# Kernel tuning notes

Hardware: AMD Instinct MI355X
Metric: run time of the kernel (lower is better)

The kernel has to match this reference:

```python
import jax, jax.numpy as jnp
import numpy as np

SEQ_LEN, BATCH, DIM = 128, 128, 1024

def setup_inputs() -> dict:
    key = jax.random.key(0)
    k1, k2, k3, k4 = jax.random.split(key, 4)
    scale = 1.0 / np.sqrt(DIM)
    return {
        "x": jax.random.normal(k1, (SEQ_LEN, BATCH, DIM), dtype=jnp.float32),
        "h0": jax.random.normal(k2, (BATCH, DIM), dtype=jnp.float32),
        "Wx": jax.random.normal(k3, (DIM, DIM), dtype=jnp.float32) * scale,
        "Wh": jax.random.normal(k4, (DIM, DIM), dtype=jnp.float32) * scale,
        "b": jnp.zeros((DIM,), dtype=jnp.float32),
    }

def reference(x, h0, Wx, Wh, b):
    # Vanilla tanh RNN cell scanned over seq_len (dropout is identity at keep_prob=1).
    # Precompute the input projection for all timesteps in one big GEMM.
    xp = jnp.einsum('sbi,ij->sbj', x, Wx) + b  # [S, B, H]
    def step(h, xp_t):
        h_new = jnp.tanh(xp_t + h @ Wh)
        return h_new, h_new
    _, hs = jax.lax.scan(step, h0, xp)
    return hs  # [seq_len, batch, hidden]: stacked hidden states
```

## Files before the change

kernel.cpp:

```cpp
#include <hip/hip_runtime.h>
#include <math.h>


#define DIM 1024
#define BATCH 128
#define SEQ 128
#define BD (BATCH * DIM)
#define NBLK 128
#define GRP 16
#define HSTR 1032
#define FLAGSTR 16
#define XNB 256
#define HXGRP 16384

typedef __attribute__((ext_vector_type(8))) short bf16x8;
typedef __attribute__((ext_vector_type(4))) float f32x4;

static __device__ __forceinline__ unsigned short f2bf_rne(float f) {
    unsigned u = __builtin_bit_cast(unsigned, f);
    unsigned r = (u + 0x7FFFu + ((u >> 16) & 1u)) >> 16;
    return (unsigned short)r;
}
static __device__ __forceinline__ float bf2f(unsigned short h) {
    return __builtin_bit_cast(float, ((unsigned)h) << 16);
}

__global__ __launch_bounds__(512) void xp_pers(
    const float* __restrict__ x,
    const float* __restrict__ Wx,
    const float* __restrict__ bias,
    float* __restrict__ out)
{
    __shared__ unsigned short hHi[16 * HSTR];
    __shared__ unsigned short hLo[16 * HSTR];
    __shared__ f32x4 redS[256];

    const int tid = threadIdx.x;
    const int bid = blockIdx.x;
    const int tg  = bid >> 7;
    const int bt  = (bid >> 4) & 7;
    const int ct  = bid & 15;
    const int B0  = bt * 16;
    const int Cb  = ct * 64;
    const int NT  = SEQ / 2;

    const int w = tid >> 6;
    const int l = tid & 63;
    const int n = l & 15;
    const int q = l >> 4;
    const int cb = Cb + (w >> 1) * 16;
    const int K0 = (w & 1) * 512;

    bf16x8 Bhi[16], Blo[16];
    #pragma unroll
    for (int s = 0; s < 16; ++s) {
        bf16x8 hi, lo;
        #pragma unroll
        for (int j = 0; j < 8; ++j) {
            const int k = K0 + 32 * s + q * 8 + j;
            const float wv = Wx[(size_t)k * DIM + cb + n];
            const unsigned short h16 = f2bf_rne(wv);
            hi[j] = (short)h16;
            lo[j] = (short)f2bf_rne(wv - bf2f(h16));
        }
        Bhi[s] = hi;
        Blo[s] = lo;
    }

    const float bv = bias[cb + n];

    const int sr = tid >> 5;
    const int su = tid & 31;

    {
        const float* xT = x + (size_t)(tg * NT) * BD + (size_t)B0 * DIM;
        const unsigned long long* srow =
            (const unsigned long long*)(xT + (size_t)sr * DIM);
        unsigned short* dh = &hHi[sr * HSTR];
        unsigned short* dl = &hLo[sr * HSTR];
        #pragma unroll
        for (int i = 0; i < 16; ++i) {
            const unsigned long long v = srow[su + 32 * i];
            const float f0 = __builtin_bit_cast(float, (unsigned)(v & 0xFFFFFFFFull));
            const float f1 = __builtin_bit_cast(float, (unsigned)(v >> 32));
            const unsigned short h0 = f2bf_rne(f0);
            const unsigned short h1 = f2bf_rne(f1);
            const unsigned short l0 = f2bf_rne(f0 - bf2f(h0));
            const unsigned short l1 = f2bf_rne(f1 - bf2f(h1));
            *(unsigned*)(dh + 2 * (su + 32 * i)) = (unsigned)h0 | ((unsigned)h1 << 16);
            *(unsigned*)(dl + 2 * (su + 32 * i)) = (unsigned)l0 | ((unsigned)l1 << 16);
        }
    }

    for (int tt = 0; tt < NT; ++tt) {
        const int t = tg * NT + tt;
        float* outT = out + (size_t)t * BD;

        __syncthreads();

        unsigned long long xr[16];
        if (tt + 1 < NT) {
            const float* xN = x + (size_t)(t + 1) * BD + (size_t)B0 * DIM;
            const unsigned long long* srow =
                (const unsigned long long*)(xN + (size_t)sr * DIM);
            #pragma unroll
            for (int i = 0; i < 16; ++i) xr[i] = srow[su + 32 * i];
        }

        f32x4 acc = {0.f, 0.f, 0.f, 0.f};
        {
            const unsigned short* rh = &hHi[(l & 15) * HSTR + K0];
            const unsigned short* rl = &hLo[(l & 15) * HSTR + K0];
            #pragma unroll
            for (int s = 0; s < 16; ++s) {
                const bf16x8 ah = *(const bf16x8*)(rh + 32 * s + 8 * q);
                const bf16x8 al = *(const bf16x8*)(rl + 32 * s + 8 * q);
                acc = __builtin_amdgcn_mfma_f32_16x16x32_bf16(ah, Bhi[s], acc, 0, 0, 0);
                acc = __builtin_amdgcn_mfma_f32_16x16x32_bf16(al, Bhi[s], acc, 0, 0, 0);
                acc = __builtin_amdgcn_mfma_f32_16x16x32_bf16(ah, Blo[s], acc, 0, 0, 0);
            }
        }

        if (w & 1) redS[(w >> 1) * 64 + l] = acc;
        __syncthreads();

        if (!(w & 1)) {
            const f32x4 p = redS[(w >> 1) * 64 + l];
            #pragma unroll
            for (int i = 0; i < 4; ++i)
                outT[(size_t)(B0 + q * 4 + i) * DIM + cb + n] = acc[i] + p[i] + bv;
        }

        if (tt + 1 < NT) {
            unsigned short* dh = &hHi[sr * HSTR];
            unsigned short* dl = &hLo[sr * HSTR];
            #pragma unroll
            for (int i = 0; i < 16; ++i) {
                const unsigned long long v = xr[i];
                const float f0 = __builtin_bit_cast(float, (unsigned)(v & 0xFFFFFFFFull));
                const float f1 = __builtin_bit_cast(float, (unsigned)(v >> 32));
                const unsigned short h0 = f2bf_rne(f0);
                const unsigned short h1 = f2bf_rne(f1);
                const unsigned short l0 = f2bf_rne(f0 - bf2f(h0));
                const unsigned short l1 = f2bf_rne(f1 - bf2f(h1));
                *(unsigned*)(dh + 2 * (su + 32 * i)) = (unsigned)h0 | ((unsigned)h1 << 16);
                *(unsigned*)(dl + 2 * (su + 32 * i)) = (unsigned)l0 | ((unsigned)l1 << 16);
            }
        }
    }
}

__global__ __launch_bounds__(512) void rnn_scan(
    const float* __restrict__ h0,
    const float* __restrict__ Wh,
    float* out,
    unsigned* flags,
    unsigned short* hX)
{
    __shared__ unsigned short hS[16 * HSTR];
    __shared__ f32x4 redS[256];

    const int tid = threadIdx.x;
    const int bid = blockIdx.x;
    const int bt  = bid >> 4;
    const int ct  = bid & 15;
    const int B0  = bt * 16;
    const int Cb  = ct * 64;

    const int w = tid >> 6;
    const int l = tid & 63;
    const int n = l & 15;
    const int q = l >> 4;
    const int cb = Cb + (w >> 1) * 16;
    const int K0 = (w & 1) * 512;

    bf16x8 Bhi[16], Blo[16];
    #pragma unroll
    for (int s = 0; s < 16; ++s) {
        bf16x8 hi, lo;
        #pragma unroll
        for (int j = 0; j < 8; ++j) {
            const int k = K0 + 32 * s + q * 8 + j;
            const float wv = Wh[(size_t)k * DIM + cb + n];
            const unsigned short h16 = f2bf_rne(wv);
            hi[j] = (short)h16;
            lo[j] = (short)f2bf_rne(wv - bf2f(h16));
        }
        Bhi[s] = hi;
        Blo[s] = lo;
    }

    const int sr = tid >> 5;
    const int su = tid & 31;
    const int qq = tid & 3;
    const int c0 = (tid >> 2) & 127;

    for (int t = 0; t < SEQ; ++t) {
        float* outT = out + (size_t)t * BD;

        float xpv[4];
        if (!(w & 1)) {
            #pragma unroll
            for (int i = 0; i < 4; ++i)
                xpv[i] = __builtin_nontemporal_load(
                    &outT[(size_t)(B0 + q * 4 + i) * DIM + cb + n]);
        }

        if (t == 0) {
            const float* hsrc = h0 + (size_t)B0 * DIM;
            const unsigned long long* srow =
                (const unsigned long long*)(hsrc + (size_t)sr * DIM);
            unsigned short* drow = &hS[sr * HSTR];
            #pragma unroll
            for (int i = 0; i < 16; ++i) {
                const unsigned long long v = srow[su + 32 * i];
                const float f0 = __builtin_bit_cast(float, (unsigned)(v & 0xFFFFFFFFull));
                const float f1 = __builtin_bit_cast(float, (unsigned)(v >> 32));
                const unsigned pk =
                    (unsigned)f2bf_rne(f0) | ((unsigned)f2bf_rne(f1) << 16);
                *(unsigned*)(drow + 2 * (su + 32 * i)) = pk;
            }
        } else {
            const unsigned short* gX = hX + (size_t)((t - 1) & 1) * (8 * HXGRP)
                                          + (size_t)bt * HXGRP;
            #pragma unroll
            for (int half = 0; half < 2; ++half) {
                const int cp = c0 + half * 128;
                unsigned long long L[4];
                #pragma unroll
                for (int cc = 0; cc < 4; ++cc)
                    L[cc] = __hip_atomic_load(
                        (const unsigned long long*)(gX + (size_t)(4 * cp + cc) * 16 + qq * 4),
                        __ATOMIC_RELAXED, __HIP_MEMORY_SCOPE_AGENT);
                #pragma unroll
                for (int i = 0; i < 2; ++i) {
                    const unsigned a0 = (unsigned)(L[0] >> (32 * i));
                    const unsigned a1 = (unsigned)(L[1] >> (32 * i));
                    const unsigned a2 = (unsigned)(L[2] >> (32 * i));
                    const unsigned a3 = (unsigned)(L[3] >> (32 * i));
                    const unsigned r0w0 = (a0 & 0xFFFFu) | (a1 << 16);
                    const unsigned r0w1 = (a2 & 0xFFFFu) | (a3 << 16);
                    const unsigned r1w0 = (a0 >> 16) | (a1 & 0xFFFF0000u);
                    const unsigned r1w1 = (a2 >> 16) | (a3 & 0xFFFF0000u);
                    *(unsigned long long*)&hS[(4 * qq + 2 * i) * HSTR + 4 * cp] =
                        (unsigned long long)r0w0 | ((unsigned long long)r0w1 << 32);
                    *(unsigned long long*)&hS[(4 * qq + 2 * i + 1) * HSTR + 4 * cp] =
                        (unsigned long long)r1w0 | ((unsigned long long)r1w1 << 32);
                }
            }
        }

        __syncthreads();

        f32x4 acc = {0.f, 0.f, 0.f, 0.f};
        {
            const unsigned short* hrow = &hS[(l & 15) * HSTR + K0];
            #pragma unroll
            for (int s = 0; s < 16; ++s) {
                const bf16x8 a = *(const bf16x8*)(hrow + 32 * s + 8 * q);
                acc = __builtin_amdgcn_mfma_f32_16x16x32_bf16(a, Bhi[s], acc, 0, 0, 0);
                acc = __builtin_amdgcn_mfma_f32_16x16x32_bf16(a, Blo[s], acc, 0, 0, 0);
            }
        }

        if (w & 1) redS[(w >> 1) * 64 + l] = acc;
        __syncthreads();

        if (!(w & 1)) {
            const f32x4 p = redS[(w >> 1) * 64 + l];
            float v0 = tanhf(acc[0] + p[0] + xpv[0]);
            float v1 = tanhf(acc[1] + p[1] + xpv[1]);
            float v2 = tanhf(acc[2] + p[2] + xpv[2]);
            float v3 = tanhf(acc[3] + p[3] + xpv[3]);

            const unsigned p0 = (unsigned)f2bf_rne(v0) | ((unsigned)f2bf_rne(v1) << 16);
            const unsigned p1 = (unsigned)f2bf_rne(v2) | ((unsigned)f2bf_rne(v3) << 16);
            unsigned short* gW = hX + (size_t)(t & 1) * (8 * HXGRP) + (size_t)bt * HXGRP;
            __hip_atomic_store(
                (unsigned long long*)(gW + (size_t)(cb + n) * 16 + q * 4),
                (unsigned long long)p0 | ((unsigned long long)p1 << 32),
                __ATOMIC_RELAXED, __HIP_MEMORY_SCOPE_AGENT);

            __builtin_nontemporal_store(v0, &outT[(size_t)(B0 + q * 4 + 0) * DIM + cb + n]);
            __builtin_nontemporal_store(v1, &outT[(size_t)(B0 + q * 4 + 1) * DIM + cb + n]);
            __builtin_nontemporal_store(v2, &outT[(size_t)(B0 + q * 4 + 2) * DIM + cb + n]);
            __builtin_nontemporal_store(v3, &outT[(size_t)(B0 + q * 4 + 3) * DIM + cb + n]);
        }

        if (t < SEQ - 1) {
            asm volatile("s_waitcnt vmcnt(0)" ::: "memory");
            __syncthreads();
            if (tid == 0)
                __hip_atomic_store(&flags[bid * FLAGSTR], (unsigned)(t + 1),
                                   __ATOMIC_RELAXED, __HIP_MEMORY_SCOPE_AGENT);
            if (tid < GRP) {
                const unsigned* slot = &flags[(bt * GRP + tid) * FLAGSTR];
                while (__hip_atomic_load(slot, __ATOMIC_RELAXED,
                                         __HIP_MEMORY_SCOPE_AGENT) < (unsigned)(t + 1))
                    __builtin_amdgcn_s_sleep(2);
            }
            __syncthreads();
        }
    }
}

extern "C" void kernel_launch(void* const* d_in, const int* in_sizes, int n_in,
                              void* d_out, int out_size, void* d_ws, size_t ws_size,
                              hipStream_t stream) {
    const float* x  = (const float*)d_in[0];
    const float* h0 = (const float*)d_in[1];
    const float* Wx = (const float*)d_in[2];
    const float* Wh = (const float*)d_in[3];
    const float* b  = (const float*)d_in[4];
    float* out = (float*)d_out;
    unsigned* flags = (unsigned*)d_ws;
    unsigned short* hX = (unsigned short*)((char*)d_ws + 8192);

    hipMemsetAsync(d_ws, 0, NBLK * FLAGSTR * sizeof(unsigned), stream);

    xp_pers<<<dim3(XNB), dim3(512), 0, stream>>>(x, Wx, b, out);

    rnn_scan<<<dim3(NBLK), dim3(512), 0, stream>>>(h0, Wh, out, flags, hX);
}
```

Before: 800.6 us.

## Fuse input projection and recurrent scan into one kernel with flag-based overlap

Merges the input-projection producer and the recurrent scan into one persistent launch of 384 blocks. The 256 projection blocks write xp timestep by timestep, interleaving timesteps between the two groups, and publish per-block progress flags. The 128 scan blocks spin on those flags before reading xp, so the projection runs underneath the sequential recurrence instead of before it. The projection's hi/lo weight split is also moved from within-wave to across wave pairs, and the scan now signals its flag before its output stores. The cost is more register pressure and dependence on all 384 blocks being co-resident; without that the spin-waits could deadlock.

```diff
diff --git a/kernel.cpp b/kernel.cpp
--- a/kernel.cpp
+++ b/kernel.cpp
@@ -6,11 +6,12 @@
 #define BATCH 128
 #define SEQ 128
 #define BD (BATCH * DIM)
-#define NBLK 128
+#define XNB 256
+#define SNB 128
+#define TNB 384
 #define GRP 16
 #define HSTR 1032
 #define FLAGSTR 16
-#define XNB 256
 #define HXGRP 16384
 
 typedef __attribute__((ext_vector_type(8))) short bf16x8;
@@ -25,281 +26,267 @@
     return __builtin_bit_cast(float, ((unsigned)h) << 16);
 }
 
-__global__ __launch_bounds__(512) void xp_pers(
+__global__ __launch_bounds__(512, 4) void rnn_fused(
     const float* __restrict__ x,
+    const float* __restrict__ h0,
     const float* __restrict__ Wx,
+    const float* __restrict__ Wh,
     const float* __restrict__ bias,
-    float* __restrict__ out)
+    float* out,
+    unsigned* scanflags,
+    unsigned* xpflags,
+    unsigned short* hX)
 {
-    __shared__ unsigned short hHi[16 * HSTR];
-    __shared__ unsigned short hLo[16 * HSTR];
+    __shared__ unsigned short smA[16 * HSTR];
+    __shared__ unsigned short smB[16 * HSTR];
     __shared__ f32x4 redS[256];
 
     const int tid = threadIdx.x;
-    const int bid = blockIdx.x;
-    const int tg  = bid >> 7;
-    const int bt  = (bid >> 4) & 7;
-    const int ct  = bid & 15;
-    const int B0  = bt * 16;
-    const int Cb  = ct * 64;
-    const int NT  = SEQ / 2;
-
+    const int gid = blockIdx.x;
     const int w = tid >> 6;
     const int l = tid & 63;
     const int n = l & 15;
     const int q = l >> 4;
-    const int cb = Cb + (w >> 1) * 16;
-    const int K0 = (w & 1) * 512;
-
-    bf16x8 Bhi[16], Blo[16];
-    #pragma unroll
-    for (int s = 0; s < 16; ++s) {
-        bf16x8 hi, lo;
-        #pragma unroll
-        for (int j = 0; j < 8; ++j) {
-            const int k = K0 + 32 * s + q * 8 + j;
-            const float wv = Wx[(size_t)k * DIM + cb + n];
-            const unsigned short h16 = f2bf_rne(wv);
-            hi[j] = (short)h16;
-            lo[j] = (short)f2bf_rne(wv - bf2f(h16));
-        }
-        Bhi[s] = hi;
-        Blo[s] = lo;
-    }
-
-    const float bv = bias[cb + n];
 
     const int sr = tid >> 5;
     const int su = tid & 31;
 
-    {
-        const float* xT = x + (size_t)(tg * NT) * BD + (size_t)B0 * DIM;
-        const unsigned long long* srow =
-            (const unsigned long long*)(xT + (size_t)sr * DIM);
-        unsigned short* dh = &hHi[sr * HSTR];
-        unsigned short* dl = &hLo[sr * HSTR];
+    if (gid < XNB) {
+        const int tg = gid >> 7;
+        const int bt = (gid >> 4) & 7;
+        const int ct = gid & 15;
+        const int B0 = bt * 16;
+        const int Cb = ct * 64;
+        const int cb = Cb + (w >> 1) * 16;
+        const int role = w & 1;
+
+        bf16x8 Bfr[32];
         #pragma unroll
-        for (int i = 0; i < 16; ++i) {
-            const unsigned long long v = srow[su + 32 * i];
-            const float f0 = __builtin_bit_cast(float, (unsigned)(v & 0xFFFFFFFFull));
-            const float f1 = __builtin_bit_cast(float, (unsigned)(v >> 32));
-            const unsigned short h0 = f2bf_rne(f0);
-            const unsigned short h1 = f2bf_rne(f1);
-            const unsigned short l0 = f2bf_rne(f0 - bf2f(h0));
-            const unsigned short l1 = f2bf_rne(f1 - bf2f(h1));
-            *(unsigned*)(dh + 2 * (su + 32 * i)) = (unsigned)h0 | ((unsigned)h1 << 16);
-            *(unsigned*)(dl + 2 * (su + 32 * i)) = (unsigned)l0 | ((unsigned)l1 << 16);
+        for (int s = 0; s < 32; ++s) {
+            bf16x8 fr;
+            #pragma unroll
+            for (int j = 0; j < 8; ++j) {
+                const int k = 32 * s + q * 8 + j;
+                const float wv = Wx[(size_t)k * DIM + cb + n];
+                const unsigned short h16 = f2bf_rne(wv);
+                fr[j] = role ? (short)f2bf_rne(wv - bf2f(h16)) : (short)h16;
+            }
+            Bfr[s] = fr;
         }
-    }
-
-    for (int tt = 0; tt < NT; ++tt) {
-        const int t = tg * NT + tt;
-        float* outT = out + (size_t)t * BD;
-
-        __syncthreads();
-
-        unsigned long long xr[16];
-        if (tt + 1 < NT) {
-            const float* xN = x + (size_t)(t + 1) * BD + (size_t)B0 * DIM;
-            const unsigned long long* srow =
-                (const unsigned long long*)(xN + (size_t)sr * DIM);
+        const float bv = bias[cb + n];
+
+        for (int tt = 0; tt < SEQ / 2; ++tt) {
+            const int t = 2 * tt + tg;
+            const float* xT = x + (size_t)t * BD + (size_t)B0 * DIM;
+            float* outT = out + (size_t)t * BD;
+
+            {
+                const unsigned long long* srow =
+                    (const unsigned long long*)(xT + (size_t)sr * DIM);
+                unsigned short* dh = &smA[sr * HSTR];
+                unsigned short* dl = &smB[sr * HSTR];
+                #pragma unroll
+                for (int i = 0; i < 16; ++i) {
+                    const unsigned long long v = srow[su + 32 * i];
+                    const float f0 = __builtin_bit_cast(float, (unsigned)(v & 0xFFFFFFFFull));
+                    const float f1 = __builtin_bit_cast(float, (unsigned)(v >> 32));
+                    const unsigned short h0v = f2bf_rne(f0);
+                    const unsigned short h1v = f2bf_rne(f1);
+                    const unsigned short l0v = f2bf_rne(f0 - bf2f(h0v));
+                    const unsigned short l1v = f2bf_rne(f1 - bf2f(h1v));
+                    *(unsigned*)(dh + 2 * (su + 32 * i)) =
+                        (unsigned)h0v | ((unsigned)h1v << 16);
+                    *(unsigned*)(dl + 2 * (su + 32 * i)) =
+                        (unsigned)l0v | ((unsigned)l1v << 16);
+                }
+            }
+            __syncthreads();
+
+            f32x4 acc = {0.f, 0.f, 0.f, 0.f};
+            {
+                const unsigned short* rh = &smA[(l & 15) * HSTR];
+                const unsigned short* rl = &smB[(l & 15) * HSTR];
+                if (!role) {
+                    #pragma unroll
+                    for (int s = 0; s < 32; ++s) {
+                        const bf16x8 ah = *(const bf16x8*)(rh + 32 * s + 8 * q);
+                        const bf16x8 al = *(const bf16x8*)(rl + 32 * s + 8 * q);
+                        acc = __builtin_amdgcn_mfma_f32_16x16x32_bf16(ah, Bfr[s], acc, 0, 0, 0);
+                        acc = __builtin_amdgcn_mfma_f32_16x16x32_bf16(al, Bfr[s], acc, 0, 0, 0);
+                    }
+                } else {
+                    #pragma unroll
+                    for (int s = 0; s < 32; ++s) {
+                        const bf16x8 ah = *(const bf16x8*)(rh + 32 * s + 8 * q);
+                        acc = __builtin_amdgcn_mfma_f32_16x16x32_bf16(ah, Bfr[s], acc, 0, 0, 0);
+                    }
+                }
+            }
+
+            if (role) redS[(w >> 1) * 64 + l] = acc;
+            __syncthreads();
+
+            if (!role) {
+                const f32x4 p = redS[(w >> 1) * 64 + l];
+                #pragma unroll
+                for (int i = 0; i < 4; ++i)
+                    __hip_atomic_store(&outT[(size_t)(B0 + q * 4 + i) * DIM + cb + n],
+                                       acc[i] + p[i] + bv,
+                                       __ATOMIC_RELAXED, __HIP_MEMORY_SCOPE_AGENT);
+            }
+
+            asm volatile("s_waitcnt vmcnt(0)" ::: "memory");
+            __syncthreads();
+            if (tid == 0)
+                __hip_atomic_store(&xpflags[gid * FLAGSTR], (unsigned)(tt + 1),
+                                   __ATOMIC_RELAXED, __HIP_MEMORY_SCOPE_AGENT);
+        }
+    } else {
+        const int bid = gid - XNB;
+        const int bt  = bid >> 4;
+        const int ct  = bid & 15;
+        const int B0  = bt * 16;
+        const int Cb  = ct * 64;
+        const int cb  = Cb + (w >> 1) * 16;
+        const int K0  = (w & 1) * 512;
+
+        bf16x8 Bhi[16], Blo[16];
+        #pragma unroll
+        for (int s = 0; s < 16; ++s) {
+            bf16x8 hi, lo;
             #pragma unroll
-            for (int i = 0; i < 16; ++i) xr[i] = srow[su + 32 * i];
+            for (int j = 0; j < 8; ++j) {
+                const int k = K0 + 32 * s + q * 8 + j;
+                const float wv = Wh[(size_t)k * DIM + cb + n];
+                const unsigned short h16 = f2bf_rne(wv);
+                hi[j] = (short)h16;
+                lo[j] = (short)f2bf_rne(wv - bf2f(h16));
+            }
+            Bhi[s] = hi;
+            Blo[s] = lo;
         }
 
-        f32x4 acc = {0.f, 0.f, 0.f, 0.f};
-        {
-            const unsigned short* rh = &hHi[(l & 15) * HSTR + K0];
-            const unsigned short* rl = &hLo[(l & 15) * HSTR + K0];
-            #pragma unroll
-            for (int s = 0; s < 16; ++s) {
-                const bf16x8 ah = *(const bf16x8*)(rh + 32 * s + 8 * q);
-                const bf16x8 al = *(const bf16x8*)(rl + 32 * s + 8 * q);
-                acc = __builtin_amdgcn_mfma_f32_16x16x32_bf16(ah, Bhi[s], acc, 0, 0, 0);
-                acc = __builtin_amdgcn_mfma_f32_16x16x32_bf16(al, Bhi[s], acc, 0, 0, 0);
-                acc = __builtin_amdgcn_mfma_f32_16x16x32_bf16(ah, Blo[s], acc, 0, 0, 0);
-            }
-        }
-
-        if (w & 1) redS[(w >> 1) * 64 + l] = acc;
-        __syncthreads();
-
-        if (!(w & 1)) {
-            const f32x4 p = redS[(w >> 1) * 64 + l];
-            #pragma unroll
-            for (int i = 0; i < 4; ++i)
-                outT[(size_t)(B0 + q * 4 + i) * DIM + cb + n] = acc[i] + p[i] + bv;
-        }
-
-        if (tt + 1 < NT) {
-            unsigned short* dh = &hHi[sr * HSTR];
-            unsigned short* dl = &hLo[sr * HSTR];
-            #pragma unroll
-            for (int i = 0; i < 16; ++i) {
-                const unsigned long long v = xr[i];
-                const float f0 = __builtin_bit_cast(float, (unsigned)(v & 0xFFFFFFFFull));
-                const float f1 = __builtin_bit_cast(float, (unsigned)(v >> 32));
-                const unsigned short h0 = f2bf_rne(f0);
-                const unsigned short h1 = f2bf_rne(f1);
-                const unsigned short l0 = f2bf_rne(f0 - bf2f(h0));
-                const unsigned short l1 = f2bf_rne(f1 - bf2f(h1));
-                *(unsigned*)(dh + 2 * (su + 32 * i)) = (unsigned)h0 | ((unsigned)h1 << 16);
-                *(unsigned*)(dl + 2 * (su + 32 * i)) = (unsigned)l0 | ((unsigned)l1 << 16);
-            }
-        }
-    }
-}
-
-__global__ __launch_bounds__(512) void rnn_scan(
-    const float* __restrict__ h0,
-    const float* __restrict__ Wh,
-    float* out,
-    unsigned* flags,
-    unsigned short* hX)
-{
-    __shared__ unsigned short hS[16 * HSTR];
-    __shared__ f32x4 redS[256];
-
-    const int tid = threadIdx.x;
-    const int bid = blockIdx.x;
-    const int bt  = bid >> 4;
-    const int ct  = bid & 15;
-    const int B0  = bt * 16;
-    const int Cb  = ct * 64;
-
-    const int w = tid >> 6;
-    const int l = tid & 63;
-    const int n = l & 15;
-    const int q = l >> 4;
-    const int cb = Cb + (w >> 1) * 16;
-    const int K0 = (w & 1) * 512;
-
-    bf16x8 Bhi[16], Blo[16];
-    #pragma unroll
-    for (int s = 0; s < 16; ++s) {
-        bf16x8 hi, lo;
-        #pragma unroll
-        for (int j = 0; j < 8; ++j) {
-            const int k = K0 + 32 * s + q * 8 + j;
-            const float wv = Wh[(size_t)k * DIM + cb + n];
-            const unsigned short h16 = f2bf_rne(wv);
-            hi[j] = (short)h16;
-            lo[j] = (short)f2bf_rne(wv - bf2f(h16));
-        }
-        Bhi[s] = hi;
-        Blo[s] = lo;
-    }
-
-    const int sr = tid >> 5;
-    const int su = tid & 31;
-    const int qq = tid & 3;
-    const int c0 = (tid >> 2) & 127;
-
-    for (int t = 0; t < SEQ; ++t) {
-        float* outT = out + (size_t)t * BD;
-
-        float xpv[4];
-        if (!(w & 1)) {
-            #pragma unroll
-            for (int i = 0; i < 4; ++i)
-                xpv[i] = __builtin_nontemporal_load(
-                    &outT[(size_t)(B0 + q * 4 + i) * DIM + cb + n]);
-        }
-
-        if (t == 0) {
-            const float* hsrc = h0 + (size_t)B0 * DIM;
-            const unsigned long long* srow =
-                (const unsigned long long*)(hsrc + (size_t)sr * DIM);
-            unsigned short* drow = &hS[sr * HSTR];
-            #pragma unroll
-            for (int i = 0; i < 16; ++i) {
-                const unsigned long long v = srow[su + 32 * i];
-                const float f0 = __builtin_bit_cast(float, (unsigned)(v & 0xFFFFFFFFull));
-                const float f1 = __builtin_bit_cast(float, (unsigned)(v >> 32));
-                const unsigned pk =
-                    (unsigned)f2bf_rne(f0) | ((unsigned)f2bf_rne(f1) << 16);
-                *(unsigned*)(drow + 2 * (su + 32 * i)) = pk;
-            }
-        } else {
-            const unsigned short* gX = hX + (size_t)((t - 1) & 1) * (8 * HXGRP)
-                                          + (size_t)bt * HXGRP;
-            #pragma unroll
-            for (int half = 0; half < 2; ++half) {
-                const int cp = c0 + half * 128;
-                unsigned long long L[4];
-                #pragma unroll
-                for (int cc = 0; cc < 4; ++cc)
-                    L[cc] = __hip_atomic_load(
-                        (const unsigned long long*)(gX + (size_t)(4 * cp + cc) * 16 + qq * 4),
+        const int qq = tid & 3;
+        const int c0 = (tid >> 2) & 127;
+
+        for (int t = 0; t < SEQ; ++t) {
+            float* outT = out + (size_t)t * BD;
+
+            float xpv[4];
+            if (!(w & 1)) {
+                const unsigned* xslot =
+                    &xpflags[(((t & 1) << 7) + bt * 16 + ct) * FLAGSTR];
+                const unsigned need = (unsigned)(t >> 1) + 1u;
+                while (__hip_atomic_load(xslot, __ATOMIC_RELAXED,
+                                         __HIP_MEMORY_SCOPE_AGENT) < need)
+                    __builtin_amdgcn_s_sleep(1);
+                #pragma unroll
+                for (int i = 0; i < 4; ++i)
+                    xpv[i] = __hip_atomic_load(
+                        &outT[(size_t)(B0 + q * 4 + i) * DIM + cb + n],
                         __ATOMIC_RELAXED, __HIP_MEMORY_SCOPE_AGENT);
-                #pragma unroll
-                for (int i = 0; i < 2; ++i) {
-                    const unsigned a0 = (unsigned)(L[0] >> (32 * i));
-                    const unsigned a1 = (unsigned)(L[1] >> (32 * i));
-                    const unsigned a2 = (unsigned)(L[2] >> (32 * i));
-                    const unsigned a3 = (unsigned)(L[3] >> (32 * i));
-                    const unsigned r0w0 = (a0 & 0xFFFFu) | (a1 << 16);
-                    const unsigned r0w1 = (a2 & 0xFFFFu) | (a3 << 16);
-                    const unsigned r1w0 = (a0 >> 16) | (a1 & 0xFFFF0000u);
-                    const unsigned r1w1 = (a2 >> 16) | (a3 & 0xFFFF0000u);
-                    *(unsigned long long*)&hS[(4 * qq + 2 * i) * HSTR + 4 * cp] =
-                        (unsigned long long)r0w0 | ((unsigned long long)r0w1 << 32);
-                    *(unsigned long long*)&hS[(4 * qq + 2 * i + 1) * HSTR + 4 * cp] =
-                        (unsigned long long)r1w0 | ((unsigned long long)r1w1 << 32);
-                }
-            }
-        }
-
-        __syncthreads();
-
-        f32x4 acc = {0.f, 0.f, 0.f, 0.f};
-        {
-            const unsigned short* hrow = &hS[(l & 15) * HSTR + K0];
-            #pragma unroll
-            for (int s = 0; s < 16; ++s) {
-                const bf16x8 a = *(const bf16x8*)(hrow + 32 * s + 8 * q);
-                acc = __builtin_amdgcn_mfma_f32_16x16x32_bf16(a, Bhi[s], acc, 0, 0, 0);
-                acc = __builtin_amdgcn_mfma_f32_16x16x32_bf16(a, Blo[s], acc, 0, 0, 0);
-            }
-        }
-
-        if (w & 1) redS[(w >> 1) * 64 + l] = acc;
-        __syncthreads();
-
-        if (!(w & 1)) {
-            const f32x4 p = redS[(w >> 1) * 64 + l];
-            float v0 = tanhf(acc[0] + p[0] + xpv[0]);
-            float v1 = tanhf(acc[1] + p[1] + xpv[1]);
-            float v2 = tanhf(acc[2] + p[2] + xpv[2]);
-            float v3 = tanhf(acc[3] + p[3] + xpv[3]);
-
-            const unsigned p0 = (unsigned)f2bf_rne(v0) | ((unsigned)f2bf_rne(v1) << 16);
-            const unsigned p1 = (unsigned)f2bf_rne(v2) | ((unsigned)f2bf_rne(v3) << 16);
-            unsigned short* gW = hX + (size_t)(t & 1) * (8 * HXGRP) + (size_t)bt * HXGRP;
-            __hip_atomic_store(
-                (unsigned long long*)(gW + (size_t)(cb + n) * 16 + q * 4),
-                (unsigned long long)p0 | ((unsigned long long)p1 << 32),
-                __ATOMIC_RELAXED, __HIP_MEMORY_SCOPE_AGENT);
-
-            __builtin_nontemporal_store(v0, &outT[(size_t)(B0 + q * 4 + 0) * DIM + cb + n]);
-            __builtin_nontemporal_store(v1, &outT[(size_t)(B0 + q * 4 + 1) * DIM + cb + n]);
-            __builtin_nontemporal_store(v2, &outT[(size_t)(B0 + q * 4 + 2) * DIM + cb + n]);
-            __builtin_nontemporal_store(v3, &outT[(size_t)(B0 + q * 4 + 3) * DIM + cb + n]);
-        }
-
-        if (t < SEQ - 1) {
-            asm volatile("s_waitcnt vmcnt(0)" ::: "memory");
-            __syncthreads();
-            if (tid == 0)
-                __hip_atomic_store(&flags[bid * FLAGSTR], (unsigned)(t + 1),
-                                   __ATOMIC_RELAXED, __HIP_MEMORY_SCOPE_AGENT);
-            if (tid < GRP) {
-                const unsigned* slot = &flags[(bt * GRP + tid) * FLAGSTR];
-                while (__hip_atomic_load(slot, __ATOMIC_RELAXED,
-                                         __HIP_MEMORY_SCOPE_AGENT) < (unsigned)(t + 1))
-                    __builtin_amdgcn_s_sleep(2);
-            }
-            __syncthreads();
+            }
+
+            if (t == 0) {
+                const float* hsrc = h0 + (size_t)B0 * DIM;
+                const unsigned long long* srow =
+                    (const unsigned long long*)(hsrc + (size_t)sr * DIM);
+                unsigned short* drow = &smA[sr * HSTR];
+                #pragma unroll
+                for (int i = 0; i < 16; ++i) {
+                    const unsigned long long v = srow[su + 32 * i];
+                    const float f0 = __builtin_bit_cast(float, (unsigned)(v & 0xFFFFFFFFull));
+                    const float f1 = __builtin_bit_cast(float, (unsigned)(v >> 32));
+                    const unsigned pk =
+                        (unsigned)f2bf_rne(f0) | ((unsigned)f2bf_rne(f1) << 16);
+                    *(unsigned*)(drow + 2 * (su + 32 * i)) = pk;
+                }
+            } else {
+                const unsigned short* gX = hX + (size_t)((t - 1) & 1) * (8 * HXGRP)
+                                              + (size_t)bt * HXGRP;
+                #pragma unroll
+                for (int half = 0; half < 2; ++half) {
+                    const int cp = c0 + half * 128;
+                    unsigned long long L[4];
+                    #pragma unroll
+                    for (int cc = 0; cc < 4; ++cc)
+                        L[cc] = __hip_atomic_load(
+                            (const unsigned long long*)(gX + (size_t)(4 * cp + cc) * 16 + qq * 4),
+                            __ATOMIC_RELAXED, __HIP_MEMORY_SCOPE_AGENT);
+                    #pragma unroll
+                    for (int i = 0; i < 2; ++i) {
+                        const unsigned a0 = (unsigned)(L[0] >> (32 * i));
+                        const unsigned a1 = (unsigned)(L[1] >> (32 * i));
+                        const unsigned a2 = (unsigned)(L[2] >> (32 * i));
+                        const unsigned a3 = (unsigned)(L[3] >> (32 * i));
+                        const unsigned r0w0 = (a0 & 0xFFFFu) | (a1 << 16);
+                        const unsigned r0w1 = (a2 & 0xFFFFu) | (a3 << 16);
+                        const unsigned r1w0 = (a0 >> 16) | (a1 & 0xFFFF0000u);
+                        const unsigned r1w1 = (a2 >> 16) | (a3 & 0xFFFF0000u);
+                        *(unsigned long long*)&smA[(4 * qq + 2 * i) * HSTR + 4 * cp] =
+                            (unsigned long long)r0w0 | ((unsigned long long)r0w1 << 32);
+                        *(unsigned long long*)&smA[(4 * qq + 2 * i + 1) * HSTR + 4 * cp] =
+                            (unsigned long long)r1w0 | ((unsigned long long)r1w1 << 32);
+                    }
+                }
+            }
+
+            __syncthreads();
+
+            f32x4 acc = {0.f, 0.f, 0.f, 0.f};
+            {
+                const unsigned short* hrow = &smA[(l & 15) * HSTR + K0];
+                #pragma unroll
+                for (int s = 0; s < 16; ++s) {
+                    const bf16x8 a = *(const bf16x8*)(hrow + 32 * s + 8 * q);
+                    acc = __builtin_amdgcn_mfma_f32_16x16x32_bf16(a, Bhi[s], acc, 0, 0, 0);
+                    acc = __builtin_amdgcn_mfma_f32_16x16x32_bf16(a, Blo[s], acc, 0, 0, 0);
+                }
+            }
+
+            if (w & 1) redS[(w >> 1) * 64 + l] = acc;
+            __syncthreads();
+
+            float v0, v1, v2, v3;
+            if (!(w & 1)) {
+                const f32x4 p = redS[(w >> 1) * 64 + l];
+                v0 = tanhf(acc[0] + p[0] + xpv[0]);
+                v1 = tanhf(acc[1] + p[1] + xpv[1]);
+                v2 = tanhf(acc[2] + p[2] + xpv[2]);
+                v3 = tanhf(acc[3] + p[3] + xpv[3]);
+                const unsigned p0 = (unsigned)f2bf_rne(v0) | ((unsigned)f2bf_rne(v1) << 16);
+                const unsigned p1 = (unsigned)f2bf_rne(v2) | ((unsigned)f2bf_rne(v3) << 16);
+                unsigned short* gW = hX + (size_t)(t & 1) * (8 * HXGRP) + (size_t)bt * HXGRP;
+                __hip_atomic_store(
+                    (unsigned long long*)(gW + (size_t)(cb + n) * 16 + q * 4),
+                    (unsigned long long)p0 | ((unsigned long long)p1 << 32),
+                    __ATOMIC_RELAXED, __HIP_MEMORY_SCOPE_AGENT);
+            }
+
+            if (t < SEQ - 1) {
+                asm volatile("s_waitcnt vmcnt(0)" ::: "memory");
+                __syncthreads();
+                if (tid == 0)
+                    __hip_atomic_store(&scanflags[bid * FLAGSTR], (unsigned)(t + 1),
+                                       __ATOMIC_RELAXED, __HIP_MEMORY_SCOPE_AGENT);
+            }
+
+            if (!(w & 1)) {
+                __builtin_nontemporal_store(v0, &outT[(size_t)(B0 + q * 4 + 0) * DIM + cb + n]);
+                __builtin_nontemporal_store(v1, &outT[(size_t)(B0 + q * 4 + 1) * DIM + cb + n]);
+                __builtin_nontemporal_store(v2, &outT[(size_t)(B0 + q * 4 + 2) * DIM + cb + n]);
+                __builtin_nontemporal_store(v3, &outT[(size_t)(B0 + q * 4 + 3) * DIM + cb + n]);
+            }
+
+            if (t < SEQ - 1) {
+                if (tid < GRP) {
+                    const unsigned* slot = &scanflags[(bt * GRP + tid) * FLAGSTR];
+                    while (__hip_atomic_load(slot, __ATOMIC_RELAXED,
+                                             __HIP_MEMORY_SCOPE_AGENT) < (unsigned)(t + 1))
+                        __builtin_amdgcn_s_sleep(1);
+                }
+                __syncthreads();
+            }
         }
     }
 }
@@ -313,12 +300,12 @@
     const float* Wh = (const float*)d_in[3];
     const float* b  = (const float*)d_in[4];
     float* out = (float*)d_out;
-    unsigned* flags = (unsigned*)d_ws;
-    unsigned short* hX = (unsigned short*)((char*)d_ws + 8192);
-
-    hipMemsetAsync(d_ws, 0, NBLK * FLAGSTR * sizeof(unsigned), stream);
-
-    xp_pers<<<dim3(XNB), dim3(512), 0, stream>>>(x, Wx, b, out);
-
-    rnn_scan<<<dim3(NBLK), dim3(512), 0, stream>>>(h0, Wh, out, flags, hX);
+    unsigned* scanflags = (unsigned*)d_ws;
+    unsigned* xpflags   = (unsigned*)((char*)d_ws + 8192);
+    unsigned short* hX  = (unsigned short*)((char*)d_ws + 24576);
+
+    hipMemsetAsync(d_ws, 0, 24576, stream);
+
+    rnn_fused<<<dim3(TNB), dim3(512), 0, stream>>>(
+        x, h0, Wx, Wh, b, out, scanflags, xpflags, hX);
 }
```

New measurement: 1.575 ms. 1.97x slower.

## Pre-split x into swizzled bf16 hi/lo slabs and remap scan block placement

Applied to the files above, without the earlier changes.

Adds a conversion kernel that splits x into bf16 hi/lo pairs laid out in swizzled 64KB slabs. A new persistent xp kernel then streams those slabs straight into shared memory with wide copies, so the per-step float-to-bf16 split disappears from the projection loop. The scan kernel remaps block indices so that batch-tile groups are interleaved across the grid. It also publishes its ready flag before the output stores and shortens the spin sleep. The new path needs a workspace of about 65MB, adds an extra pass over x, and falls back to the old kernel when the workspace is too small.

```diff
diff --git a/kernel.cpp b/kernel.cpp
--- a/kernel.cpp
+++ b/kernel.cpp
@@ -12,6 +12,8 @@
 #define FLAGSTR 16
 #define XNB 256
 #define HXGRP 16384
+#define XW_OFF (1u << 20)
+#define XW_BYTES (64u << 20)
 
 typedef __attribute__((ext_vector_type(8))) short bf16x8;
 typedef __attribute__((ext_vector_type(4))) float f32x4;
@@ -23,6 +25,142 @@
 }
 static __device__ __forceinline__ float bf2f(unsigned short h) {
     return __builtin_bit_cast(float, ((unsigned)h) << 16);
+}
+
+__global__ __launch_bounds__(256) void xcv(
+    const float* __restrict__ x, unsigned short* __restrict__ xw)
+{
+    const int blk = blockIdx.x;
+    const int t  = blk >> 3;
+    const int bt = blk & 7;
+    const float* src = x + (size_t)t * BD + (size_t)bt * 16 * DIM;
+    char* slab = (char*)xw + (size_t)blk * 65536;
+    const int tid = threadIdx.x;
+
+    #pragma unroll
+    for (int uu = 0; uu < 8; ++uu) {
+        const int u = tid + uu * 256;
+        const int row = u >> 7;
+        const int cb8 = u & 127;
+        const float4 a = *(const float4*)&src[(size_t)row * DIM + cb8 * 8];
+        const float4 c = *(const float4*)&src[(size_t)row * DIM + cb8 * 8 + 4];
+        const float f[8] = {a.x, a.y, a.z, a.w, c.x, c.y, c.z, c.w};
+        unsigned hh[8], ll[8];
+        #pragma unroll
+        for (int j = 0; j < 8; ++j) {
+            const unsigned short h = f2bf_rne(f[j]);
+            hh[j] = h;
+            ll[j] = f2bf_rne(f[j] - bf2f(h));
+        }
+        uint4 hv, lv;
+        hv.x = hh[0] | (hh[1] << 16);  hv.y = hh[2] | (hh[3] << 16);
+        hv.z = hh[4] | (hh[5] << 16);  hv.w = hh[6] | (hh[7] << 16);
+        lv.x = ll[0] | (ll[1] << 16);  lv.y = ll[2] | (ll[3] << 16);
+        lv.z = ll[4] | (ll[5] << 16);  lv.w = ll[6] | (ll[7] << 16);
+        const size_t off = (size_t)row * 2048
+                         + (size_t)(((unsigned)(cb8 << 4)) ^ (unsigned)((row & 7) << 4));
+        *(uint4*)(slab + off) = hv;
+        *(uint4*)(slab + off + 32768) = lv;
+    }
+}
+
+__global__ __launch_bounds__(512) void xp_fast(
+    const unsigned short* __restrict__ xw,
+    const float* __restrict__ Wx,
+    const float* __restrict__ bias,
+    float* __restrict__ out)
+{
+    __shared__ char xbuf[65536];
+    __shared__ f32x4 redS[256];
+
+    const int tid = threadIdx.x;
+    const int p = blockIdx.x;
+    const int g = p & 7;
+    const int slot = p >> 3;
+    const int idx = g + 8 * (slot >> 4);
+    const int ct = slot & 15;
+    const int tg = idx >> 3;
+    const int bt = idx & 7;
+    const int B0 = bt * 16;
+    const int Cb = ct * 64;
+
+    const int w = tid >> 6;
+    const int l = tid & 63;
+    const int n = l & 15;
+    const int q = l >> 4;
+    const int cb = Cb + (w >> 1) * 16;
+    const int K0 = (w & 1) * 512;
+
+    bf16x8 Bhi[16], Blo[16];
+    #pragma unroll
+    for (int s = 0; s < 16; ++s) {
+        bf16x8 hi, lo;
+        #pragma unroll
+        for (int j = 0; j < 8; ++j) {
+            const int k = K0 + 32 * s + q * 8 + j;
+            const float wv = Wx[(size_t)k * DIM + cb + n];
+            const unsigned short h16 = f2bf_rne(wv);
+            hi[j] = (short)h16;
+            lo[j] = (short)f2bf_rne(wv - bf2f(h16));
+        }
+        Bhi[s] = hi;
+        Blo[s] = lo;
+    }
+    const float bv = bias[cb + n];
+
+    const int t0 = tg * 64;
+    const unsigned swzr = (unsigned)((l & 7) << 4);
+    const char* hb = xbuf + (size_t)(l & 15) * 2048;
+
+    uint4 xr[8];
+    {
+        const char* slab = (const char*)xw + (size_t)(t0 * 8 + bt) * 65536;
+        #pragma unroll
+        for (int r = 0; r < 8; ++r)
+            xr[r] = *(const uint4*)(slab + tid * 16 + r * 8192);
+        #pragma unroll
+        for (int r = 0; r < 8; ++r)
+            *(uint4*)(xbuf + tid * 16 + r * 8192) = xr[r];
+    }
+
+    for (int tt = 0; tt < 64; ++tt) {
+        __syncthreads();
+
+        if (tt + 1 < 64) {
+            const char* slab = (const char*)xw + (size_t)((t0 + tt + 1) * 8 + bt) * 65536;
+            #pragma unroll
+            for (int r = 0; r < 8; ++r)
+                xr[r] = *(const uint4*)(slab + tid * 16 + r * 8192);
+        }
+
+        f32x4 acc = {0.f, 0.f, 0.f, 0.f};
+        #pragma unroll
+        for (int s = 0; s < 16; ++s) {
+            const int off = (int)(((unsigned)(K0 * 2 + 64 * s + 16 * q)) ^ swzr);
+            const bf16x8 ah = *(const bf16x8*)(hb + off);
+            const bf16x8 al = *(const bf16x8*)(hb + off + 32768);
+            acc = __builtin_amdgcn_mfma_f32_16x16x32_bf16(ah, Bhi[s], acc, 0, 0, 0);
+            acc = __builtin_amdgcn_mfma_f32_16x16x32_bf16(al, Bhi[s], acc, 0, 0, 0);
+            acc = __builtin_amdgcn_mfma_f32_16x16x32_bf16(ah, Blo[s], acc, 0, 0, 0);
+        }
+
+        if (w & 1) redS[(w >> 1) * 64 + l] = acc;
+        __syncthreads();
+
+        if (!(w & 1)) {
+            const f32x4 pr = redS[(w >> 1) * 64 + l];
+            float* outT = out + (size_t)(t0 + tt) * BD;
+            #pragma unroll
+            for (int i = 0; i < 4; ++i)
+                outT[(size_t)(B0 + q * 4 + i) * DIM + cb + n] = acc[i] + pr[i] + bv;
+        }
+
+        if (tt + 1 < 64) {
+            #pragma unroll
+            for (int r = 0; r < 8; ++r)
+                *(uint4*)(xbuf + tid * 16 + r * 8192) = xr[r];
+        }
+    }
 }
 
 __global__ __launch_bounds__(512) void xp_pers(
@@ -66,7 +204,6 @@
         Bhi[s] = hi;
         Blo[s] = lo;
     }
-
     const float bv = bias[cb + n];
 
     const int sr = tid >> 5;
@@ -74,8 +211,7 @@
 
     {
         const float* xT = x + (size_t)(tg * NT) * BD + (size_t)B0 * DIM;
-        const unsigned long long* srow =
-            (const unsigned long long*)(xT + (size_t)sr * DIM);
+        const unsigned long long* srow = (const unsigned long long*)(xT + (size_t)sr * DIM);
         unsigned short* dh = &hHi[sr * HSTR];
         unsigned short* dl = &hLo[sr * HSTR];
         #pragma unroll
@@ -101,8 +237,7 @@
         unsigned long long xr[16];
         if (tt + 1 < NT) {
             const float* xN = x + (size_t)(t + 1) * BD + (size_t)B0 * DIM;
-            const unsigned long long* srow =
-                (const unsigned long long*)(xN + (size_t)sr * DIM);
+            const unsigned long long* srow = (const unsigned long long*)(xN + (size_t)sr * DIM);
             #pragma unroll
             for (int i = 0; i < 16; ++i) xr[i] = srow[su + 32 * i];
         }
@@ -161,9 +296,10 @@
     __shared__ f32x4 redS[256];
 
     const int tid = threadIdx.x;
-    const int bid = blockIdx.x;
-    const int bt  = bid >> 4;
-    const int ct  = bid & 15;
+    const int p   = blockIdx.x;
+    const int bt  = p & 7;
+    const int ct  = p >> 3;
+    const int lbid = bt * 16 + ct;
     const int B0  = bt * 16;
     const int Cb  = ct * 64;
 
@@ -266,13 +402,13 @@
         if (w & 1) redS[(w >> 1) * 64 + l] = acc;
         __syncthreads();
 
+        float v0, v1, v2, v3;
         if (!(w & 1)) {
-            const f32x4 p = redS[(w >> 1) * 64 + l];
-            float v0 = tanhf(acc[0] + p[0] + xpv[0]);
-            float v1 = tanhf(acc[1] + p[1] + xpv[1]);
-            float v2 = tanhf(acc[2] + p[2] + xpv[2]);
-            float v3 = tanhf(acc[3] + p[3] + xpv[3]);
-
+            const f32x4 pp = redS[(w >> 1) * 64 + l];
+            v0 = tanhf(acc[0] + pp[0] + xpv[0]);
+            v1 = tanhf(acc[1] + pp[1] + xpv[1]);
+            v2 = tanhf(acc[2] + pp[2] + xpv[2]);
+            v3 = tanhf(acc[3] + pp[3] + xpv[3]);
             const unsigned p0 = (unsigned)f2bf_rne(v0) | ((unsigned)f2bf_rne(v1) << 16);
             const unsigned p1 = (unsigned)f2bf_rne(v2) | ((unsigned)f2bf_rne(v3) << 16);
             unsigned short* gW = hX + (size_t)(t & 1) * (8 * HXGRP) + (size_t)bt * HXGRP;
@@ -280,7 +416,17 @@
                 (unsigned long long*)(gW + (size_t)(cb + n) * 16 + q * 4),
                 (unsigned long long)p0 | ((unsigned long long)p1 << 32),
                 __ATOMIC_RELAXED, __HIP_MEMORY_SCOPE_AGENT);
-
+        }
+
+        if (t < SEQ - 1) {
+            asm volatile("s_waitcnt vmcnt(0)" ::: "memory");
+            __syncthreads();
+            if (tid == 0)
+                __hip_atomic_store(&flags[lbid * FLAGSTR], (unsigned)(t + 1),
+                                   __ATOMIC_RELAXED, __HIP_MEMORY_SCOPE_AGENT);
+        }
+
+        if (!(w & 1)) {
             __builtin_nontemporal_store(v0, &outT[(size_t)(B0 + q * 4 + 0) * DIM + cb + n]);
             __builtin_nontemporal_store(v1, &outT[(size_t)(B0 + q * 4 + 1) * DIM + cb + n]);
             __builtin_nontemporal_store(v2, &outT[(size_t)(B0 + q * 4 + 2) * DIM + cb + n]);
@@ -288,16 +434,11 @@
         }
 
         if (t < SEQ - 1) {
-            asm volatile("s_waitcnt vmcnt(0)" ::: "memory");
-            __syncthreads();
-            if (tid == 0)
-                __hip_atomic_store(&flags[bid * FLAGSTR], (unsigned)(t + 1),
-                                   __ATOMIC_RELAXED, __HIP_MEMORY_SCOPE_AGENT);
             if (tid < GRP) {
                 const unsigned* slot = &flags[(bt * GRP + tid) * FLAGSTR];
                 while (__hip_atomic_load(slot, __ATOMIC_RELAXED,
                                          __HIP_MEMORY_SCOPE_AGENT) < (unsigned)(t + 1))
-                    __builtin_amdgcn_s_sleep(2);
+                    __builtin_amdgcn_s_sleep(1);
             }
             __syncthreads();
         }
@@ -315,10 +456,16 @@
     float* out = (float*)d_out;
     unsigned* flags = (unsigned*)d_ws;
     unsigned short* hX = (unsigned short*)((char*)d_ws + 8192);
+    unsigned short* xw = (unsigned short*)((char*)d_ws + XW_OFF);
 
     hipMemsetAsync(d_ws, 0, NBLK * FLAGSTR * sizeof(unsigned), stream);
 
-    xp_pers<<<dim3(XNB), dim3(512), 0, stream>>>(x, Wx, b, out);
+    if (ws_size >= (size_t)XW_OFF + (size_t)XW_BYTES) {
+        xcv<<<dim3(1024), dim3(256), 0, stream>>>(x, xw);
+        xp_fast<<<dim3(XNB), dim3(512), 0, stream>>>(xw, Wx, b, out);
+    } else {
+        xp_pers<<<dim3(XNB), dim3(512), 0, stream>>>(x, Wx, b, out);
+    }
 
     rnn_scan<<<dim3(NBLK), dim3(512), 0, stream>>>(h0, Wh, out, flags, hX);
 }
```

Measured after the change: 1.011 ms. 1.26x slower.

## Signal per-wave flag increments, remap block indices, and cheapen hi/lo split

Applied to the files above, without the earlier changes.

The scan kernel no longer waits for the whole block before publishing its flag. Each writer wave now drains its own stores and atomically increments the block's counter, and consumers wait for four increments per step with a shorter sleep. Block-to-tile mappings in both kernels are permuted, likely to spread groups across chiplets or XCDs. The hi/lo bf16 split of x now truncates the high half instead of rounding, which changes the numerics slightly but keeps hi+lo accurate. A barrier in the xp kernel moves after the prefetch loads, and the flag counters must start at zero for the increments to be correct.

```diff
diff --git a/kernel.cpp b/kernel.cpp
--- a/kernel.cpp
+++ b/kernel.cpp
@@ -25,6 +25,19 @@
     return __builtin_bit_cast(float, ((unsigned)h) << 16);
 }
 
+static __device__ __forceinline__ void split_pair(
+    unsigned long long v, unsigned& hp, unsigned& lp)
+{
+    const unsigned u0 = (unsigned)v;
+    const unsigned u1 = (unsigned)(v >> 32);
+    const float f0 = __builtin_bit_cast(float, u0);
+    const float f1 = __builtin_bit_cast(float, u1);
+    hp = (u0 >> 16) | (u1 & 0xFFFF0000u);
+    const float r0 = f0 - __builtin_bit_cast(float, u0 & 0xFFFF0000u);
+    const float r1 = f1 - __builtin_bit_cast(float, u1 & 0xFFFF0000u);
+    lp = (unsigned)f2bf_rne(r0) | ((unsigned)f2bf_rne(r1) << 16);
+}
+
 __global__ __launch_bounds__(512) void xp_pers(
     const float* __restrict__ x,
     const float* __restrict__ Wx,
@@ -37,9 +50,10 @@
 
     const int tid = threadIdx.x;
     const int bid = blockIdx.x;
-    const int tg  = bid >> 7;
-    const int bt  = (bid >> 4) & 7;
-    const int ct  = bid & 15;
+    const int g   = bid & 15;
+    const int ct  = bid >> 4;
+    const int tg  = g >> 3;
+    const int bt  = g & 7;
     const int B0  = bt * 16;
     const int Cb  = ct * 64;
     const int NT  = SEQ / 2;
@@ -66,7 +80,6 @@
         Bhi[s] = hi;
         Blo[s] = lo;
     }
-
     const float bv = bias[cb + n];
 
     const int sr = tid >> 5;
@@ -80,23 +93,16 @@
         unsigned short* dl = &hLo[sr * HSTR];
         #pragma unroll
         for (int i = 0; i < 16; ++i) {
-            const unsigned long long v = srow[su + 32 * i];
-            const float f0 = __builtin_bit_cast(float, (unsigned)(v & 0xFFFFFFFFull));
-            const float f1 = __builtin_bit_cast(float, (unsigned)(v >> 32));
-            const unsigned short h0 = f2bf_rne(f0);
-            const unsigned short h1 = f2bf_rne(f1);
-            const unsigned short l0 = f2bf_rne(f0 - bf2f(h0));
-            const unsigned short l1 = f2bf_rne(f1 - bf2f(h1));
-            *(unsigned*)(dh + 2 * (su + 32 * i)) = (unsigned)h0 | ((unsigned)h1 << 16);
-            *(unsigned*)(dl + 2 * (su + 32 * i)) = (unsigned)l0 | ((unsigned)l1 << 16);
+            unsigned hp, lp;
+            split_pair(srow[su + 32 * i], hp, lp);
+            *(unsigned*)(dh + 2 * (su + 32 * i)) = hp;
+            *(unsigned*)(dl + 2 * (su + 32 * i)) = lp;
         }
     }
 
     for (int tt = 0; tt < NT; ++tt) {
         const int t = tg * NT + tt;
         float* outT = out + (size_t)t * BD;
-
-        __syncthreads();
 
         unsigned long long xr[16];
         if (tt + 1 < NT) {
@@ -106,6 +112,8 @@
             #pragma unroll
             for (int i = 0; i < 16; ++i) xr[i] = srow[su + 32 * i];
         }
+
+        __syncthreads();
 
         f32x4 acc = {0.f, 0.f, 0.f, 0.f};
         {
@@ -136,15 +144,10 @@
             unsigned short* dl = &hLo[sr * HSTR];
             #pragma unroll
             for (int i = 0; i < 16; ++i) {
-                const unsigned long long v = xr[i];
-                const float f0 = __builtin_bit_cast(float, (unsigned)(v & 0xFFFFFFFFull));
-                const float f1 = __builtin_bit_cast(float, (unsigned)(v >> 32));
-                const unsigned short h0 = f2bf_rne(f0);
-                const unsigned short h1 = f2bf_rne(f1);
-                const unsigned short l0 = f2bf_rne(f0 - bf2f(h0));
-                const unsigned short l1 = f2bf_rne(f1 - bf2f(h1));
-                *(unsigned*)(dh + 2 * (su + 32 * i)) = (unsigned)h0 | ((unsigned)h1 << 16);
-                *(unsigned*)(dl + 2 * (su + 32 * i)) = (unsigned)l0 | ((unsigned)l1 << 16);
+                unsigned hp, lp;
+                split_pair(xr[i], hp, lp);
+                *(unsigned*)(dh + 2 * (su + 32 * i)) = hp;
+                *(unsigned*)(dl + 2 * (su + 32 * i)) = lp;
             }
         }
     }
@@ -161,9 +164,10 @@
     __shared__ f32x4 redS[256];
 
     const int tid = threadIdx.x;
-    const int bid = blockIdx.x;
-    const int bt  = bid >> 4;
-    const int ct  = bid & 15;
+    const int p   = blockIdx.x;
+    const int bt  = p & 7;
+    const int ct  = p >> 3;
+    const int lbid = bt * 16 + ct;
     const int B0  = bt * 16;
     const int Cb  = ct * 64;
 
@@ -267,11 +271,11 @@
         __syncthreads();
 
         if (!(w & 1)) {
-            const f32x4 p = redS[(w >> 1) * 64 + l];
-            float v0 = tanhf(acc[0] + p[0] + xpv[0]);
-            float v1 = tanhf(acc[1] + p[1] + xpv[1]);
-            float v2 = tanhf(acc[2] + p[2] + xpv[2]);
-            float v3 = tanhf(acc[3] + p[3] + xpv[3]);
+            const f32x4 pp = redS[(w >> 1) * 64 + l];
+            const float v0 = tanhf(acc[0] + pp[0] + xpv[0]);
+            const float v1 = tanhf(acc[1] + pp[1] + xpv[1]);
+            const float v2 = tanhf(acc[2] + pp[2] + xpv[2]);
+            const float v3 = tanhf(acc[3] + pp[3] + xpv[3]);
 
             const unsigned p0 = (unsigned)f2bf_rne(v0) | ((unsigned)f2bf_rne(v1) << 16);
             const unsigned p1 = (unsigned)f2bf_rne(v2) | ((unsigned)f2bf_rne(v3) << 16);
@@ -281,6 +285,13 @@
                 (unsigned long long)p0 | ((unsigned long long)p1 << 32),
                 __ATOMIC_RELAXED, __HIP_MEMORY_SCOPE_AGENT);
 
+            if (t < SEQ - 1) {
+                asm volatile("s_waitcnt vmcnt(0)" ::: "memory");
+                if (l == 0)
+                    __hip_atomic_fetch_add(&flags[lbid * FLAGSTR], 1u,
+                                           __ATOMIC_RELAXED, __HIP_MEMORY_SCOPE_AGENT);
+            }
+
             __builtin_nontemporal_store(v0, &outT[(size_t)(B0 + q * 4 + 0) * DIM + cb + n]);
             __builtin_nontemporal_store(v1, &outT[(size_t)(B0 + q * 4 + 1) * DIM + cb + n]);
             __builtin_nontemporal_store(v2, &outT[(size_t)(B0 + q * 4 + 2) * DIM + cb + n]);
@@ -288,16 +299,12 @@
         }
 
         if (t < SEQ - 1) {
-            asm volatile("s_waitcnt vmcnt(0)" ::: "memory");
-            __syncthreads();
-            if (tid == 0)
-                __hip_atomic_store(&flags[bid * FLAGSTR], (unsigned)(t + 1),
-                                   __ATOMIC_RELAXED, __HIP_MEMORY_SCOPE_AGENT);
             if (tid < GRP) {
+                const unsigned need = 4u * (unsigned)(t + 1);
                 const unsigned* slot = &flags[(bt * GRP + tid) * FLAGSTR];
                 while (__hip_atomic_load(slot, __ATOMIC_RELAXED,
-                                         __HIP_MEMORY_SCOPE_AGENT) < (unsigned)(t + 1))
-                    __builtin_amdgcn_s_sleep(2);
+                                         __HIP_MEMORY_SCOPE_AGENT) < need)
+                    __builtin_amdgcn_s_sleep(1);
             }
             __syncthreads();
         }
```

After: 871.0 us. 1.09x slower.
